# Kernel optimization log

Measured on AMD Instinct MI355X. Metric: run time of the kernel, lower is better.

## Reference

```python
import jax, jax.numpy as jnp
import numpy as np

EPS = 1e-12

def _l2(v):
    return v / (jnp.linalg.norm(v) + EPS)

def _sn_weight(w, u):
    # Spectral normalization, one power iteration with stored u (not updated here).
    cout = w.shape[-1]
    wm = w.reshape(-1, cout)              # [d, cout]
    u = jax.lax.stop_gradient(u)
    v = _l2(wm @ u)                       # [d]
    u2 = _l2(wm.T @ v)                    # [cout]
    sigma = v @ (wm @ u2)
    return w / sigma

def _conv1x1(x, w, u):
    # 1x1 conv, no bias, with spectral-normalized kernel. x: [B,H,W,Cin], w: [1,1,Cin,Cout]
    wbar = _sn_weight(w, u)[0, 0]         # [Cin, Cout]
    return jnp.einsum('bhwc,co->bhwo', x, wbar)

def _maxpool2(x):
    # 2x2 max pool, stride 2, valid. x: [B,H,W,C]
    B, H, W, C = x.shape
    return x.reshape(B, H // 2, 2, W // 2, 2, C).max(axis=(2, 4))

def setup_inputs() -> dict:
    key = jax.random.key(0)
    ks = jax.random.split(key, 9)
    B, H, W, C = 16, 64, 64, 64
    inp = {
        'x': jax.random.normal(ks[0], (B, H, W, C), jnp.float32),
        'w_theta': jax.random.normal(ks[1], (1, 1, C, C // 8), jnp.float32) * 0.05,
        'u_theta': jax.random.normal(ks[2], (C // 8,), jnp.float32),
        'w_phi': jax.random.normal(ks[3], (1, 1, C, C // 8), jnp.float32) * 0.05,
        'u_phi': jax.random.normal(ks[4], (C // 8,), jnp.float32),
        'w_g': jax.random.normal(ks[5], (1, 1, C, C // 2), jnp.float32) * 0.05,
        'u_g': jax.random.normal(ks[6], (C // 2,), jnp.float32),
        'w_o': jax.random.normal(ks[7], (1, 1, C // 2, C), jnp.float32) * 0.05,
        'u_o': jax.random.normal(ks[8], (C,), jnp.float32),
        'gamma': jnp.zeros((1,), jnp.float32),
    }
    return inp

def reference(x, w_theta, u_theta, w_phi, u_phi, w_g, u_g, w_o, u_o, gamma):
    B, H, W, C = x.shape
    theta = _conv1x1(x, w_theta, u_theta).reshape(B, H * W, C // 8)          # [B,HW,C/8]
    phi = _maxpool2(_conv1x1(x, w_phi, u_phi)).reshape(B, H * W // 4, C // 8)  # [B,HW/4,C/8]
    attn = jax.nn.softmax(jnp.einsum('bnk,bmk->bnm', theta, phi), axis=-1)   # [B,HW,HW/4]
    g = _maxpool2(_conv1x1(x, w_g, u_g)).reshape(B, H * W // 4, C // 2)      # [B,HW/4,C/2]
    attn_g = jnp.einsum('bnm,bmc->bnc', attn, g).reshape(B, H, W, C // 2)    # [B,H,W,C/2]
    attn_g = _conv1x1(attn_g, w_o, u_o)                                      # [B,H,W,C]
    return x + gamma * attn_g
```

## Files before the change

kernel.cpp:

```cpp
#include <hip/hip_runtime.h>
#include <hip/hip_bf16.h>
#include <math.h>

#define NB 16
#define NPIX 4096
#define MPOOL 1024

typedef __attribute__((ext_vector_type(8))) short bf16x8;
typedef __attribute__((ext_vector_type(4))) float f32x4;

__device__ inline unsigned short f2bf(float f) {
    __hip_bfloat16 h = __float2bfloat16(f);
    return *reinterpret_cast<unsigned short*>(&h);
}


__device__ inline float wave_sum64(float v) {
    #pragma unroll
    for (int off = 32; off >= 1; off >>= 1) v += __shfl_xor(v, off);
    return v;
}

__global__ void sn_kernel(const float* __restrict__ w_theta, const float* __restrict__ u_theta,
                          const float* __restrict__ w_phi,   const float* __restrict__ u_phi,
                          const float* __restrict__ w_g,     const float* __restrict__ u_g,
                          const float* __restrict__ w_o,     const float* __restrict__ u_o,
                          unsigned short* __restrict__ wcT_bf,
                          unsigned short* __restrict__ woT_bf) {
    const float* w; const float* u; unsigned short* dst; int d, cout;
    switch (blockIdx.x) {
      case 0:  w = w_theta; u = u_theta; dst = wcT_bf;           d = 64; cout = 8;  break;
      case 1:  w = w_phi;   u = u_phi;   dst = wcT_bf + 8 * 64;  d = 64; cout = 8;  break;
      case 2:  w = w_g;     u = u_g;     dst = wcT_bf + 16 * 64; d = 64; cout = 32; break;
      default: w = w_o;     u = u_o;     dst = woT_bf;           d = 32; cout = 64; break;
    }
    __shared__ float sv[64];
    __shared__ float su2[64];
    const int tid = threadIdx.x;

    float vi = 0.f;
    if (tid < d) for (int j = 0; j < cout; ++j) vi += w[tid * cout + j] * u[j];
    float nn = wave_sum64(vi * vi);
    vi *= 1.0f / (sqrtf(nn) + 1e-12f);
    sv[tid] = vi;
    __syncthreads();

    float u2j = 0.f;
    if (tid < cout) for (int i = 0; i < d; ++i) u2j += w[i * cout + tid] * sv[i];
    float nn2 = wave_sum64(u2j * u2j);
    u2j *= 1.0f / (sqrtf(nn2) + 1e-12f);
    su2[tid] = u2j;
    __syncthreads();

    float ti = 0.f;
    if (tid < d) for (int j = 0; j < cout; ++j) ti += w[tid * cout + j] * su2[j];
    float sig = wave_sum64(vi * ti);
    const float inv_sig = 1.0f / sig;
    for (int idx = tid; idx < d * cout; idx += 64) {
        const int i = idx / cout, j = idx - i * cout;
        dst[j * d + i] = f2bf(w[idx] * inv_sig);
    }
}

__global__ __launch_bounds__(256) void conv_all_kernel(const float* __restrict__ x,
                                                       const unsigned short* __restrict__ wcT_bf,
                                                       unsigned short* __restrict__ theta_bf,
                                                       unsigned short* __restrict__ phi_bf,
                                                       unsigned short* __restrict__ gT_bf) {
    __shared__ unsigned short sx[128 * 72];
    __shared__ unsigned short sw[48 * 72];

    const int tid = threadIdx.x;
    const int b  = blockIdx.x >> 5;
    const int hp = blockIdx.x & 31;
    const int h0 = hp * 2;

    const float4* xb4 = (const float4*)(x + (((size_t)b * NPIX) + h0 * 64) * 64);
    #pragma unroll
    for (int it = 0; it < 8; ++it) {
        const int li = tid + it * 256;
        float4 v = xb4[li];
        const int px = li >> 4, c4 = li & 15;
        unsigned lo = (unsigned)f2bf(v.x) | ((unsigned)f2bf(v.y) << 16);
        unsigned hi = (unsigned)f2bf(v.z) | ((unsigned)f2bf(v.w) << 16);
        uint2 pk; pk.x = lo; pk.y = hi;
        *(uint2*)(&sx[px * 72 + c4 * 4]) = pk;
    }
    for (int idx = tid; idx < 48 * 64; idx += 256) {
        const int col = idx >> 6, k = idx & 63;
        sw[col * 72 + k] = wcT_bf[idx];
    }
    __syncthreads();

    const int w    = tid >> 6;
    const int lane = tid & 63;
    const int quad = lane >> 4;
    const int lcol = lane & 15;
    const int w0   = w * 16;

    bf16x8 a[2][2];
    #pragma unroll
    for (int hh = 0; hh < 2; ++hh)
        #pragma unroll
        for (int kc = 0; kc < 2; ++kc)
            a[hh][kc] = *(const bf16x8*)(sx + (hh * 64 + w0 + lcol) * 72 + kc * 32 + quad * 8);

    f32x4 acc[2][3];
    #pragma unroll
    for (int ct = 0; ct < 3; ++ct) {
        bf16x8 b0 = *(const bf16x8*)(sw + (ct * 16 + lcol) * 72 + 0 * 32 + quad * 8);
        bf16x8 b1 = *(const bf16x8*)(sw + (ct * 16 + lcol) * 72 + 1 * 32 + quad * 8);
        #pragma unroll
        for (int hh = 0; hh < 2; ++hh) {
            f32x4 c = __builtin_amdgcn_mfma_f32_16x16x32_bf16(a[hh][0], b0, (f32x4)0.0f, 0, 0, 0);
            acc[hh][ct] = __builtin_amdgcn_mfma_f32_16x16x32_bf16(a[hh][1], b1, c, 0, 0, 0);
        }
    }

    if (lcol < 8) {
        #pragma unroll
        for (int hh = 0; hh < 2; ++hh) {
            const size_t rowbase = (size_t)b * NPIX + (h0 + hh) * 64 + w0 + quad * 4;
            #pragma unroll
            for (int r = 0; r < 4; ++r)
                theta_bf[(rowbase + r) * 8 + lcol] = f2bf(acc[hh][0][r]);
        }
    }
    const int mcb = hp * 32 + (w0 >> 1) + quad * 2;
    if (lcol >= 8) {
        #pragma unroll
        for (int r2 = 0; r2 < 2; ++r2) {
            float pe = fmaxf(fmaxf(acc[0][0][2 * r2], acc[0][0][2 * r2 + 1]),
                             fmaxf(acc[1][0][2 * r2], acc[1][0][2 * r2 + 1]));
            phi_bf[((size_t)b * MPOOL + mcb + r2) * 8 + (lcol - 8)] = f2bf(pe);
        }
    }
    #pragma unroll
    for (int ct = 1; ct < 3; ++ct) {
        const int cg = (ct - 1) * 16 + lcol;
        #pragma unroll
        for (int r2 = 0; r2 < 2; ++r2) {
            float pe = fmaxf(fmaxf(acc[0][ct][2 * r2], acc[0][ct][2 * r2 + 1]),
                             fmaxf(acc[1][ct][2 * r2], acc[1][ct][2 * r2 + 1]));
            gT_bf[((size_t)b * 32 + cg) * MPOOL + mcb + r2] = f2bf(pe);
        }
    }
}

__global__ __launch_bounds__(512) void attn_kernel(const unsigned short* __restrict__ theta_bf,
                                                   const unsigned short* __restrict__ phi_bf,
                                                   const unsigned short* __restrict__ gT_bf,
                                                   const unsigned short* __restrict__ woT_bf,
                                                   const float* __restrict__ x,
                                                   const float* __restrict__ gamma,
                                                   float* __restrict__ out) {
    __shared__ unsigned short sphi[MPOOL * 8];
    __shared__ unsigned short sg[2][32 * 264];
    __shared__ unsigned short sP[8][16 * 88];
    __shared__ unsigned short swo[64 * 40];

    const int tid  = threadIdx.x;
    const int b    = blockIdx.x >> 5;
    const int qb   = blockIdx.x & 31;
    const int w    = tid >> 6;
    const int lane = tid & 63;
    const int quad = lane >> 4;
    const int lcol = lane & 15;

    {
        const float4* src = (const float4*)(phi_bf + (size_t)b * (MPOOL * 8));
        float4* dst = (float4*)sphi;
        dst[2 * tid]     = src[2 * tid];
        dst[2 * tid + 1] = src[2 * tid + 1];
    }
    for (int idx = tid; idx < 64 * 32; idx += 512) {
        const int n = idx >> 5, k = idx & 31;
        swo[n * 40 + k] = woT_bf[idx];
    }
    const unsigned short* gTb = gT_bf + (size_t)b * (32 * MPOOL);
    const int prow = tid >> 4, pseg = tid & 15;
    {
        const float4* src = (const float4*)(gTb + prow * MPOOL + pseg * 16);
        float4 r0 = src[0], r1 = src[1];
        float4* dst = (float4*)(&sg[0][prow * 264 + pseg * 16]);
        dst[0] = r0; dst[1] = r1;
    }
    const int q0w = qb * 128 + w * 16;
    bf16x8 tfrag = (bf16x8)(short)0;
    if (quad == 0)
        tfrag = *(const bf16x8*)(theta_bf + ((size_t)b * NPIX + q0w + lcol) * 8);
    __syncthreads();

    f32x4 olo = (f32x4)0.0f, ohi = (f32x4)0.0f;
    float ls0 = 0.f, ls1 = 0.f, ls2 = 0.f, ls3 = 0.f;
    unsigned short* sPw = sP[w];
    const int wr0 = (quad * 4) * 88 + lcol;

    float4 pre0, pre1;
    for (int t = 0; t < 4; ++t) {
        if (t < 3) {
            const float4* src = (const float4*)(gTb + prow * MPOOL + (t + 1) * 256 + pseg * 16);
            pre0 = src[0]; pre1 = src[1];
        }
        const unsigned short* sgb = sg[t & 1];
        for (int cb = 0; cb < 4; ++cb) {
            const int m0 = t * 256 + cb * 64;
            f32x4 s[4];
            #pragma unroll
            for (int sc = 0; sc < 4; ++sc) {
                bf16x8 pf = *(const bf16x8*)(sphi + (size_t)(m0 + sc * 16 + lcol) * 8);
                s[sc] = __builtin_amdgcn_mfma_f32_16x16x32_bf16(tfrag, pf, (f32x4)0.0f, 0, 0, 0);
            }
            #pragma unroll
            for (int sc = 0; sc < 4; ++sc) {
                float e0 = __expf(s[sc][0]);
                float e1 = __expf(s[sc][1]);
                float e2 = __expf(s[sc][2]);
                float e3 = __expf(s[sc][3]);
                ls0 += e0; ls1 += e1; ls2 += e2; ls3 += e3;
                sPw[wr0 + sc * 16 +   0] = f2bf(e0);
                sPw[wr0 + sc * 16 +  88] = f2bf(e1);
                sPw[wr0 + sc * 16 + 176] = f2bf(e2);
                sPw[wr0 + sc * 16 + 264] = f2bf(e3);
            }
            asm volatile("s_waitcnt lgkmcnt(0)" ::: "memory");
            #pragma unroll
            for (int pk = 0; pk < 2; ++pk) {
                bf16x8 afrag = *(const bf16x8*)(sPw + lcol * 88 + pk * 32 + quad * 8);
                bf16x8 bg0 = *(const bf16x8*)(sgb + lcol * 264 + cb * 64 + pk * 32 + quad * 8);
                olo = __builtin_amdgcn_mfma_f32_16x16x32_bf16(afrag, bg0, olo, 0, 0, 0);
                bf16x8 bg1 = *(const bf16x8*)(sgb + (16 + lcol) * 264 + cb * 64 + pk * 32 + quad * 8);
                ohi = __builtin_amdgcn_mfma_f32_16x16x32_bf16(afrag, bg1, ohi, 0, 0, 0);
            }
        }
        if (t < 3) {
            float4* dst = (float4*)(&sg[(t + 1) & 1][prow * 264 + pseg * 16]);
            dst[0] = pre0; dst[1] = pre1;
        }
        __syncthreads();
    }

    #pragma unroll
    for (int off = 1; off < 16; off <<= 1) {
        ls0 += __shfl_xor(ls0, off);
        ls1 += __shfl_xor(ls1, off);
        ls2 += __shfl_xor(ls2, off);
        ls3 += __shfl_xor(ls3, off);
    }
    const float inv[4] = {1.f / ls0, 1.f / ls1, 1.f / ls2, 1.f / ls3};

    #pragma unroll
    for (int r = 0; r < 4; ++r) {
        sPw[(quad * 4 + r) * 40 + lcol]      = f2bf(olo[r] * inv[r]);
        sPw[(quad * 4 + r) * 40 + 16 + lcol] = f2bf(ohi[r] * inv[r]);
    }
    asm volatile("s_waitcnt lgkmcnt(0)" ::: "memory");
    bf16x8 agf = *(const bf16x8*)(sPw + lcol * 40 + quad * 8);

    const float gm = gamma[0];
    #pragma unroll
    for (int ct = 0; ct < 4; ++ct) {
        bf16x8 wb = *(const bf16x8*)(swo + (ct * 16 + lcol) * 40 + quad * 8);
        f32x4 oc = __builtin_amdgcn_mfma_f32_16x16x32_bf16(agf, wb, (f32x4)0.0f, 0, 0, 0);
        #pragma unroll
        for (int r = 0; r < 4; ++r) {
            const size_t idx = ((size_t)b * NPIX + q0w + quad * 4 + r) * 64 + ct * 16 + lcol;
            out[idx] = x[idx] + gm * oc[r];
        }
    }
}

extern "C" void kernel_launch(void* const* d_in, const int* in_sizes, int n_in,
                              void* d_out, int out_size, void* d_ws, size_t ws_size,
                              hipStream_t stream) {
    const float* x       = (const float*)d_in[0];
    const float* w_theta = (const float*)d_in[1];
    const float* u_theta = (const float*)d_in[2];
    const float* w_phi   = (const float*)d_in[3];
    const float* u_phi   = (const float*)d_in[4];
    const float* w_g     = (const float*)d_in[5];
    const float* u_g     = (const float*)d_in[6];
    const float* w_o     = (const float*)d_in[7];
    const float* u_o     = (const float*)d_in[8];
    const float* gamma   = (const float*)d_in[9];
    float* out = (float*)d_out;

    unsigned short* u16base  = (unsigned short*)d_ws;
    unsigned short* wcT_bf   = u16base;
    unsigned short* woT_bf   = u16base + 3072;
    unsigned short* theta_bf = u16base + 5120;
    unsigned short* phi_bf   = u16base + 529408;
    unsigned short* gT_bf    = u16base + 660480;

    sn_kernel<<<4, 64, 0, stream>>>(w_theta, u_theta, w_phi, u_phi, w_g, u_g, w_o, u_o,
                                    wcT_bf, woT_bf);
    conv_all_kernel<<<512, 256, 0, stream>>>(x, wcT_bf, theta_bf, phi_bf, gT_bf);
    attn_kernel<<<512, 512, 0, stream>>>(theta_bf, phi_bf, gT_bf, woT_bf, x, gamma, out);
}
```

Before: 122.7 us.

## Transpose score MFMA layout to pack P writes and vectorize epilogue I/O

Swaps the MFMA operand order for the QK scores so that each lane holds four consecutive keys of a single query. That lets the exp'd probabilities go to LDS as one packed 8-byte store instead of four scalar stores. The row-sum shrinks to a single accumulator reduced with two shuffles, and the P tile pitch drops from 88 to 72. Softmax normalization is now deferred and folded into the gamma scale. The output projection is also transposed so that x is read and out is written as float4. The trade-off is that the unnormalized attention output is rounded to bf16 before scaling, a small precision change.

```diff
diff --git a/kernel.cpp b/kernel.cpp
--- a/kernel.cpp
+++ b/kernel.cpp
@@ -156,7 +156,7 @@
                                                    float* __restrict__ out) {
     __shared__ unsigned short sphi[MPOOL * 8];
     __shared__ unsigned short sg[2][32 * 264];
-    __shared__ unsigned short sP[8][16 * 88];
+    __shared__ unsigned short sP[8][16 * 72];
     __shared__ unsigned short swo[64 * 40];
 
     const int tid  = threadIdx.x;
@@ -192,9 +192,8 @@
     __syncthreads();
 
     f32x4 olo = (f32x4)0.0f, ohi = (f32x4)0.0f;
-    float ls0 = 0.f, ls1 = 0.f, ls2 = 0.f, ls3 = 0.f;
+    float ls = 0.f;
     unsigned short* sPw = sP[w];
-    const int wr0 = (quad * 4) * 88 + lcol;
 
     float4 pre0, pre1;
     for (int t = 0; t < 4; ++t) {
@@ -209,7 +208,7 @@
             #pragma unroll
             for (int sc = 0; sc < 4; ++sc) {
                 bf16x8 pf = *(const bf16x8*)(sphi + (size_t)(m0 + sc * 16 + lcol) * 8);
-                s[sc] = __builtin_amdgcn_mfma_f32_16x16x32_bf16(tfrag, pf, (f32x4)0.0f, 0, 0, 0);
+                s[sc] = __builtin_amdgcn_mfma_f32_16x16x32_bf16(pf, tfrag, (f32x4)0.0f, 0, 0, 0);
             }
             #pragma unroll
             for (int sc = 0; sc < 4; ++sc) {
@@ -217,19 +216,19 @@
                 float e1 = __expf(s[sc][1]);
                 float e2 = __expf(s[sc][2]);
                 float e3 = __expf(s[sc][3]);
-                ls0 += e0; ls1 += e1; ls2 += e2; ls3 += e3;
-                sPw[wr0 + sc * 16 +   0] = f2bf(e0);
-                sPw[wr0 + sc * 16 +  88] = f2bf(e1);
-                sPw[wr0 + sc * 16 + 176] = f2bf(e2);
-                sPw[wr0 + sc * 16 + 264] = f2bf(e3);
+                ls += (e0 + e1) + (e2 + e3);
+                uint2 pk2;
+                pk2.x = (unsigned)f2bf(e0) | ((unsigned)f2bf(e1) << 16);
+                pk2.y = (unsigned)f2bf(e2) | ((unsigned)f2bf(e3) << 16);
+                *(uint2*)(sPw + lcol * 72 + sc * 16 + quad * 4) = pk2;
             }
             asm volatile("s_waitcnt lgkmcnt(0)" ::: "memory");
             #pragma unroll
-            for (int pk = 0; pk < 2; ++pk) {
-                bf16x8 afrag = *(const bf16x8*)(sPw + lcol * 88 + pk * 32 + quad * 8);
-                bf16x8 bg0 = *(const bf16x8*)(sgb + lcol * 264 + cb * 64 + pk * 32 + quad * 8);
+            for (int pkk = 0; pkk < 2; ++pkk) {
+                bf16x8 afrag = *(const bf16x8*)(sPw + lcol * 72 + pkk * 32 + quad * 8);
+                bf16x8 bg0 = *(const bf16x8*)(sgb + lcol * 264 + cb * 64 + pkk * 32 + quad * 8);
                 olo = __builtin_amdgcn_mfma_f32_16x16x32_bf16(afrag, bg0, olo, 0, 0, 0);
-                bf16x8 bg1 = *(const bf16x8*)(sgb + (16 + lcol) * 264 + cb * 64 + pk * 32 + quad * 8);
+                bf16x8 bg1 = *(const bf16x8*)(sgb + (16 + lcol) * 264 + cb * 64 + pkk * 32 + quad * 8);
                 ohi = __builtin_amdgcn_mfma_f32_16x16x32_bf16(afrag, bg1, ohi, 0, 0, 0);
             }
         }
@@ -240,33 +239,31 @@
         __syncthreads();
     }
 
-    #pragma unroll
-    for (int off = 1; off < 16; off <<= 1) {
-        ls0 += __shfl_xor(ls0, off);
-        ls1 += __shfl_xor(ls1, off);
-        ls2 += __shfl_xor(ls2, off);
-        ls3 += __shfl_xor(ls3, off);
-    }
-    const float inv[4] = {1.f / ls0, 1.f / ls1, 1.f / ls2, 1.f / ls3};
+    ls += __shfl_xor(ls, 16);
+    ls += __shfl_xor(ls, 32);
+    const float invq = 1.0f / ls;
 
     #pragma unroll
     for (int r = 0; r < 4; ++r) {
-        sPw[(quad * 4 + r) * 40 + lcol]      = f2bf(olo[r] * inv[r]);
-        sPw[(quad * 4 + r) * 40 + 16 + lcol] = f2bf(ohi[r] * inv[r]);
+        sPw[(quad * 4 + r) * 40 + lcol]      = f2bf(olo[r]);
+        sPw[(quad * 4 + r) * 40 + 16 + lcol] = f2bf(ohi[r]);
     }
     asm volatile("s_waitcnt lgkmcnt(0)" ::: "memory");
     bf16x8 agf = *(const bf16x8*)(sPw + lcol * 40 + quad * 8);
 
-    const float gm = gamma[0];
+    const float gmi = gamma[0] * invq;
+    const size_t pixbase = ((size_t)b * NPIX + q0w + lcol) * 64;
     #pragma unroll
     for (int ct = 0; ct < 4; ++ct) {
-        bf16x8 wb = *(const bf16x8*)(swo + (ct * 16 + lcol) * 40 + quad * 8);
-        f32x4 oc = __builtin_amdgcn_mfma_f32_16x16x32_bf16(agf, wb, (f32x4)0.0f, 0, 0, 0);
-        #pragma unroll
-        for (int r = 0; r < 4; ++r) {
-            const size_t idx = ((size_t)b * NPIX + q0w + quad * 4 + r) * 64 + ct * 16 + lcol;
-            out[idx] = x[idx] + gm * oc[r];
-        }
+        bf16x8 wa = *(const bf16x8*)(swo + (ct * 16 + lcol) * 40 + quad * 8);
+        f32x4 oc = __builtin_amdgcn_mfma_f32_16x16x32_bf16(wa, agf, (f32x4)0.0f, 0, 0, 0);
+        const float4 xv = *(const float4*)(x + pixbase + ct * 16 + quad * 4);
+        float4 ov;
+        ov.x = xv.x + gmi * oc[0];
+        ov.y = xv.y + gmi * oc[1];
+        ov.z = xv.z + gmi * oc[2];
+        ov.w = xv.w + gmi * oc[3];
+        *(float4*)(out + pixbase + ct * 16 + quad * 4) = ov;
     }
 }
 
```

Result: no change. 120.5 us (-1.8%).
